# Performance work log

Measured on AMD Instinct MI355X. Metric: run time of the kernel, lower is better.

The kernel has to match this reference:

```python
import jax, jax.numpy as jnp
import numpy as np

EMB = 1024
HEADS = 16
HD = EMB // HEADS

def setup_inputs() -> dict:
    key = jax.random.key(0)
    ks = jax.random.split(key, 9)
    s = 1.0 / np.sqrt(EMB)
    x = jax.random.normal(ks[0], (4, 2048, EMB), dtype=jnp.float32)
    Wq = jax.random.uniform(ks[1], (EMB, EMB), jnp.float32, -s, s)
    bq = jax.random.uniform(ks[2], (EMB,), jnp.float32, -s, s)
    Wk = jax.random.uniform(ks[3], (EMB, EMB), jnp.float32, -s, s)
    bk = jax.random.uniform(ks[4], (EMB,), jnp.float32, -s, s)
    Wv = jax.random.uniform(ks[5], (EMB, EMB), jnp.float32, -s, s)
    bv = jax.random.uniform(ks[6], (EMB,), jnp.float32, -s, s)
    Wo = jax.random.uniform(ks[7], (EMB, EMB), jnp.float32, -s, s)
    bo = jax.random.uniform(ks[8], (EMB,), jnp.float32, -s, s)
    return {"x": x, "Wq": Wq, "bq": bq, "Wk": Wk, "bk": bk, "Wv": Wv, "bv": bv, "Wo": Wo, "bo": bo}

def reference(x, Wq, bq, Wk, bk, Wv, bv, Wo, bo):
    B, T, C = x.shape
    # projections (torch Linear: y = x @ W^T + b)
    q = (x @ Wq.T + bq).reshape(B, T, HEADS, HD).transpose(0, 2, 1, 3)  # [B,H,T,hd]
    k = (x @ Wk.T + bk).reshape(B, T, HEADS, HD).transpose(0, 2, 1, 3)
    v = (x @ Wv.T + bv).reshape(B, T, HEADS, HD).transpose(0, 2, 1, 3)
    scores = jnp.einsum('bhqd,bhkd->bhqk', q, k) / jnp.sqrt(jnp.float32(HD))
    weights = jax.nn.softmax(scores, axis=-1)
    attn = jnp.einsum('bhqk,bhkd->bhqd', weights, v)
    out = attn.transpose(0, 2, 1, 3).reshape(B, T, C)
    return out @ Wo.T + bo
```

## Files before the change

kernel.cpp:

```cpp
#include <hip/hip_runtime.h>

#define TSEQ  2048
#define BATCH 4
#define NHEAD 16
#define EMB   1024

typedef __attribute__((ext_vector_type(8))) __bf16 bf16x8;
typedef __attribute__((ext_vector_type(4))) __bf16 bf16x4;
typedef __attribute__((ext_vector_type(4))) float  floatx4;

__device__ __forceinline__ void gload_lds16(const __bf16* g, __bf16* lds_uniform_base) {
  __builtin_amdgcn_global_load_lds(
      (__attribute__((address_space(1))) void*)(g),
      (__attribute__((address_space(3))) void*)(lds_uniform_base),
      16, 0, 0);
}

__global__ __launch_bounds__(256) void cvt_f32_bf16(
    const float* __restrict__ src, __bf16* __restrict__ dst)
{
  const int gid = (blockIdx.x * 256 + threadIdx.x) * 4;
  const float4 v = *(const float4*)(src + gid);
  dst[gid + 0] = (__bf16)v.x;
  dst[gid + 1] = (__bf16)v.y;
  dst[gid + 2] = (__bf16)v.z;
  dst[gid + 3] = (__bf16)v.w;
}

__global__ __launch_bounds__(256) void cvt_w4(
    const float* __restrict__ s0, const float* __restrict__ s1,
    const float* __restrict__ s2, const float* __restrict__ s3,
    __bf16* __restrict__ d0, __bf16* __restrict__ d1,
    __bf16* __restrict__ d2, __bf16* __restrict__ d3)
{
  const int z = blockIdx.z;
  const float* src = (z == 0) ? s0 : (z == 1) ? s1 : (z == 2) ? s2 : s3;
  __bf16*      dst = (z == 0) ? d0 : (z == 1) ? d1 : (z == 2) ? d2 : d3;
  const int gid = (blockIdx.x * 256 + threadIdx.x) * 4;
  const float4 v = *(const float4*)(src + gid);
  dst[gid + 0] = (__bf16)v.x;
  dst[gid + 1] = (__bf16)v.y;
  dst[gid + 2] = (__bf16)v.z;
  dst[gid + 3] = (__bf16)v.w;
}

__global__ __launch_bounds__(256) void gemm_bt_bias(
    const __bf16* __restrict__ A,
    const __bf16* __restrict__ W0, const __bf16* __restrict__ W1, const __bf16* __restrict__ W2,
    const float* __restrict__ B0, const float* __restrict__ B1, const float* __restrict__ B2,
    __bf16* __restrict__ C0, __bf16* __restrict__ C1, __bf16* __restrict__ C2)
{
  const int z = blockIdx.z;
  const __bf16* W  = (z == 0) ? W0 : ((z == 1) ? W1 : W2);
  const float*  Bb = (z == 0) ? B0 : ((z == 1) ? B1 : B2);
  __bf16*       C  = (z == 0) ? C0 : ((z == 1) ? C1 : C2);
  const float  scl = (z == 0) ? 0.125f * 1.44269504088896340736f : 1.0f;

  const int tid  = threadIdx.x;
  const int lane = tid & 63;
  const int wid  = tid >> 6;
  const int l16  = lane & 15;
  const int quad = lane >> 4;
  const int wm   = wid & 1;
  const int wn   = wid >> 1;
  const int m0   = blockIdx.y * 128;
  const int n0   = blockIdx.x * 128;

  __shared__ alignas(16) __bf16 As[128 * 32];
  __shared__ alignas(16) __bf16 Bs[128 * 32];

  floatx4 acc[4][4];
#pragma unroll
  for (int i = 0; i < 4; i++)
#pragma unroll
    for (int j = 0; j < 4; j++) acc[i][j] = (floatx4){0.f, 0.f, 0.f, 0.f};

  const int srow = tid >> 2;
  const int sseg = tid & 3;

  for (int k0 = 0; k0 < 1024; k0 += 32) {
    __syncthreads();
#pragma unroll
    for (int is = 0; is < 2; is++) {
      const int row = is * 64 + srow;
      gload_lds16(A + (size_t)(m0 + row) * 1024 + k0 + sseg * 8,
                  &As[(is * 256 + wid * 64) * 8]);
      gload_lds16(W + (size_t)(n0 + row) * 1024 + k0 + sseg * 8,
                  &Bs[(is * 256 + wid * 64) * 8]);
    }
    __syncthreads();

    bf16x8 af[4], bfr[4];
#pragma unroll
    for (int i = 0; i < 4; i++) {
      af[i]  = *(const bf16x8*)(&As[(wm * 64 + i * 16 + l16) * 32 + quad * 8]);
      bfr[i] = *(const bf16x8*)(&Bs[(wn * 64 + i * 16 + l16) * 32 + quad * 8]);
    }
#pragma unroll
    for (int i = 0; i < 4; i++)
#pragma unroll
      for (int j = 0; j < 4; j++)
        acc[i][j] = __builtin_amdgcn_mfma_f32_16x16x32_bf16(af[i], bfr[j], acc[i][j], 0, 0, 0);
  }

  float bv[4];
#pragma unroll
  for (int j = 0; j < 4; j++) bv[j] = Bb[n0 + wn * 64 + j * 16 + l16];

#pragma unroll
  for (int i = 0; i < 4; i++) {
    const size_t mrow = (size_t)m0 + wm * 64 + i * 16 + quad * 4;
#pragma unroll
    for (int j = 0; j < 4; j++) {
      const int col = n0 + wn * 64 + j * 16 + l16;
#pragma unroll
      for (int r = 0; r < 4; r++)
        C[(mrow + r) * 1024 + col] = (__bf16)((acc[i][j][r] + bv[j]) * scl);
    }
  }
}

__global__ __launch_bounds__(256) void gemm_bt_bias_f32(
    const __bf16* __restrict__ A, const __bf16* __restrict__ W,
    const float* __restrict__ Bb, float* __restrict__ C)
{
  const int tid  = threadIdx.x;
  const int lane = tid & 63;
  const int wid  = tid >> 6;
  const int l16  = lane & 15;
  const int quad = lane >> 4;
  const int wm   = wid & 1;
  const int wn   = wid >> 1;
  const int m0   = blockIdx.y * 128;
  const int n0   = blockIdx.x * 128;

  __shared__ alignas(16) __bf16 As[128 * 32];
  __shared__ alignas(16) __bf16 Bs[128 * 32];

  floatx4 acc[4][4];
#pragma unroll
  for (int i = 0; i < 4; i++)
#pragma unroll
    for (int j = 0; j < 4; j++) acc[i][j] = (floatx4){0.f, 0.f, 0.f, 0.f};

  const int srow = tid >> 2;
  const int sseg = tid & 3;

  for (int k0 = 0; k0 < 1024; k0 += 32) {
    __syncthreads();
#pragma unroll
    for (int is = 0; is < 2; is++) {
      const int row = is * 64 + srow;
      gload_lds16(A + (size_t)(m0 + row) * 1024 + k0 + sseg * 8,
                  &As[(is * 256 + wid * 64) * 8]);
      gload_lds16(W + (size_t)(n0 + row) * 1024 + k0 + sseg * 8,
                  &Bs[(is * 256 + wid * 64) * 8]);
    }
    __syncthreads();

    bf16x8 af[4], bfr[4];
#pragma unroll
    for (int i = 0; i < 4; i++) {
      af[i]  = *(const bf16x8*)(&As[(wm * 64 + i * 16 + l16) * 32 + quad * 8]);
      bfr[i] = *(const bf16x8*)(&Bs[(wn * 64 + i * 16 + l16) * 32 + quad * 8]);
    }
#pragma unroll
    for (int i = 0; i < 4; i++)
#pragma unroll
      for (int j = 0; j < 4; j++)
        acc[i][j] = __builtin_amdgcn_mfma_f32_16x16x32_bf16(af[i], bfr[j], acc[i][j], 0, 0, 0);
  }

  float bv[4];
#pragma unroll
  for (int j = 0; j < 4; j++) bv[j] = Bb[n0 + wn * 64 + j * 16 + l16];

#pragma unroll
  for (int i = 0; i < 4; i++) {
    const size_t mrow = (size_t)m0 + wm * 64 + i * 16 + quad * 4;
#pragma unroll
    for (int j = 0; j < 4; j++) {
      const int col = n0 + wn * 64 + j * 16 + l16;
#pragma unroll
      for (int r = 0; r < 4; r++)
        C[(mrow + r) * 1024 + col] = acc[i][j][r] + bv[j];
    }
  }
}

__global__ __launch_bounds__(256) void v_transpose(
    const __bf16* __restrict__ V, __bf16* __restrict__ VT)
{
  const int t0 = blockIdx.x * 64;
  const int bh = blockIdx.y;
  const int b  = bh >> 4;
  const int h  = bh & 15;
  const int tid = threadIdx.x;

  __shared__ alignas(16) __bf16 Ls[64 * 72];

  const int row = tid >> 2, seg = tid & 3;
  const __bf16* src = V + ((size_t)(b * TSEQ + t0 + row)) * EMB + h * 64;
  *(bf16x8*)(&Ls[row * 72 + seg * 8])       = *(const bf16x8*)(src + seg * 8);
  *(bf16x8*)(&Ls[row * 72 + (seg + 4) * 8]) = *(const bf16x8*)(src + (seg + 4) * 8);
  __syncthreads();

  const int od = tid >> 2, oseg = tid & 3;
  bf16x8 o0, o1;
#pragma unroll
  for (int j = 0; j < 8; j++) o0[j] = Ls[(oseg * 16 + j) * 72 + od];
#pragma unroll
  for (int j = 0; j < 8; j++) o1[j] = Ls[(oseg * 16 + 8 + j) * 72 + od];
  __bf16* dst = VT + ((size_t)bh * 64 + od) * TSEQ + t0 + oseg * 16;
  *(bf16x8*)(dst)     = o0;
  *(bf16x8*)(dst + 8) = o1;
}

#define FA_STEP(BUF, WRPTR, DO_WR, DO_LD, LDTILE)                                        \
  {                                                                                      \
    if (DO_WR) *(bf16x8*)(WRPTR) = sv;                                                   \
    if (DO_LD) sv = *(const bf16x8*)(sptr0 + (size_t)(LDTILE) * sstep);                  \
    _Pragma("unroll")                                                                    \
    for (int kg = 0; kg < 2; kg++) {                                                     \
      const bf16x8 kf0 = *(const bf16x8*)(&Ks[BUF][(kg * 16 + l16) * 72 + quad * 8]);    \
      const bf16x8 kf1 = *(const bf16x8*)(&Ks[BUF][(kg * 16 + l16) * 72 + 32 + quad * 8]); \
      floatx4 t = (floatx4){0.f, 0.f, 0.f, 0.f};                                         \
      t = __builtin_amdgcn_mfma_f32_16x16x32_bf16(kf0, qf[0], t, 0, 0, 0);               \
      t = __builtin_amdgcn_mfma_f32_16x16x32_bf16(kf1, qf[1], t, 0, 0, 0);               \
      bf16x4 pk;                                                                         \
      float ps = 0.f;                                                                    \
      _Pragma("unroll")                                                                  \
      for (int r = 0; r < 4; r++) {                                                      \
        const float p = __builtin_amdgcn_exp2f(t[r]);                                    \
        ps += p;                                                                         \
        pk[r] = (__bf16)p;                                                               \
      }                                                                                  \
      l_r += ps;                                                                         \
      *(bf16x4*)(&Pb[wid][l16 * 40 + kg * 16 + quad * 4]) = pk;                          \
    }                                                                                    \
    __asm__ __volatile__("s_waitcnt lgkmcnt(0)" ::: "memory");                           \
    {                                                                                    \
      const bf16x8 pf = *(const bf16x8*)(&Pb[wid][l16 * 40 + quad * 8]);                 \
      _Pragma("unroll")                                                                  \
      for (int dg = 0; dg < 4; dg++) {                                                   \
        const bf16x8 vf = *(const bf16x8*)(&VTs[BUF][(dg * 16 + l16) * 40 + quad * 8]);  \
        Oacc[dg] = __builtin_amdgcn_mfma_f32_16x16x32_bf16(vf, pf, Oacc[dg], 0, 0, 0);   \
      }                                                                                  \
    }                                                                                    \
    __syncthreads();                                                                     \
  }

__global__ __launch_bounds__(512, 8) void flash_attn(
    const __bf16* __restrict__ Q, const __bf16* __restrict__ K,
    const __bf16* __restrict__ VT, __bf16* __restrict__ O)
{
  const int qt   = blockIdx.x;
  const int bh   = blockIdx.y;
  const int b    = bh >> 4;
  const int h    = bh & 15;
  const int tid  = threadIdx.x;
  const int wid  = tid >> 6;
  const int lane = tid & 63;
  const int l16  = lane & 15;
  const int quad = lane >> 4;

  __shared__ alignas(16) __bf16 Ks[2][32 * 72];
  __shared__ alignas(16) __bf16 VTs[2][64 * 40];
  __shared__ alignas(16) __bf16 Pb[8][16 * 40];

  const size_t base = ((size_t)b * TSEQ) * EMB + (size_t)h * 64;
  const __bf16* qptr  = Q + base;
  const __bf16* kptr  = K + base;
  const __bf16* vtptr = VT + (size_t)bh * 64 * TSEQ;
  __bf16*       optr  = O + base;

  const int qb = qt * 128 + wid * 16;

  bf16x8 qf[2];
#pragma unroll
  for (int hf = 0; hf < 2; hf++)
    qf[hf] = *(const bf16x8*)(qptr + (size_t)(qb + l16) * EMB + hf * 32 + quad * 8);

  floatx4 Oacc[4];
#pragma unroll
  for (int dg = 0; dg < 4; dg++) Oacc[dg] = (floatx4){0.f, 0.f, 0.f, 0.f};
  float l_r = 0.f;

  const bool isK = (tid < 256);
  const int t2   = tid & 255;
  const int krow = t2 >> 3, kseg = t2 & 7;
  const int vd   = t2 >> 2, vseg = t2 & 3;

  const __bf16* sptr0;
  size_t sstep;
  __bf16 *wr0, *wr1;
  if (isK) {
    sptr0 = kptr + (size_t)krow * EMB + kseg * 8;
    sstep = (size_t)32 * EMB;
    wr0 = &Ks[0][krow * 72 + kseg * 8];
    wr1 = &Ks[1][krow * 72 + kseg * 8];
  } else {
    sptr0 = vtptr + (size_t)vd * TSEQ + vseg * 8;
    sstep = 32;
    wr0 = &VTs[0][vd * 40 + vseg * 8];
    wr1 = &VTs[1][vd * 40 + vseg * 8];
  }

  bf16x8 sv = *(const bf16x8*)(sptr0);
  *(bf16x8*)wr0 = sv;
  sv = *(const bf16x8*)(sptr0 + sstep);
  __syncthreads();

  for (int kt = 0; kt < TSEQ / 32; kt += 2) {
    FA_STEP(0, wr1, true,                  kt + 2 < TSEQ / 32, kt + 2);
    FA_STEP(1, wr0, kt + 2 < TSEQ / 32,    kt + 3 < TSEQ / 32, kt + 3);
  }

  float l = l_r;
  l += __shfl_xor(l, 16);
  l += __shfl_xor(l, 32);
  const float inv = 1.0f / l;
#pragma unroll
  for (int dg = 0; dg < 4; dg++) {
    bf16x4 ov;
#pragma unroll
    for (int r = 0; r < 4; r++) ov[r] = (__bf16)(Oacc[dg][r] * inv);
    *(bf16x4*)(optr + (size_t)(qb + l16) * EMB + dg * 16 + quad * 4) = ov;
  }
}

extern "C" void kernel_launch(void* const* d_in, const int* in_sizes, int n_in,
                              void* d_out, int out_size, void* d_ws, size_t ws_size,
                              hipStream_t stream) {
  const float* x  = (const float*)d_in[0];
  const float* Wq = (const float*)d_in[1];
  const float* bq = (const float*)d_in[2];
  const float* Wk = (const float*)d_in[3];
  const float* bk = (const float*)d_in[4];
  const float* Wv = (const float*)d_in[5];
  const float* bv = (const float*)d_in[6];
  const float* Wo = (const float*)d_in[7];
  const float* bo = (const float*)d_in[8];
  float* out = (float*)d_out;

  const size_t NELEM = (size_t)BATCH * TSEQ * EMB;
  const size_t WELEM = (size_t)EMB * EMB;

  __bf16* q_b  = (__bf16*)d_out;
  __bf16* k_b  = q_b + NELEM;
  __bf16* x_b  = (__bf16*)d_ws;
  __bf16* v_b  = x_b + NELEM;
  __bf16* wq_b = v_b + NELEM;
  __bf16* wk_b = wq_b + WELEM;
  __bf16* wv_b = wk_b + WELEM;
  __bf16* wo_b = wv_b + WELEM;

  dim3 blk(256, 1, 1);

  cvt_f32_bf16<<<(int)(NELEM / 1024), blk, 0, stream>>>(x, x_b);
  cvt_w4<<<dim3((int)(WELEM / 1024), 1, 4), blk, 0, stream>>>(
      Wq, Wk, Wv, Wo, wq_b, wk_b, wv_b, wo_b);

  gemm_bt_bias<<<dim3(8, 64, 3), blk, 0, stream>>>(
      x_b, wq_b, wk_b, wv_b, bq, bk, bv, q_b, k_b, v_b);

  v_transpose<<<dim3(TSEQ / 64, BATCH * NHEAD), blk, 0, stream>>>(v_b, x_b);

  flash_attn<<<dim3(TSEQ / 128, BATCH * NHEAD), dim3(512, 1, 1), 0, stream>>>(
      q_b, k_b, x_b, v_b);

  gemm_bt_bias_f32<<<dim3(8, 64, 1), blk, 0, stream>>>(v_b, wo_b, bo, out);
}
```

Baseline: 315.0 us.

## Double KV tile to 64 and pass P through permlane swaps instead of LDS

Each loop step now covers 64 keys instead of 32. That halves the number of barriers and lets every thread stage one K and one V^T vector per tile. The softmax probabilities are no longer written to a per-wave LDS buffer and read back. Instead, permlane32/permlane16 swaps rearrange the score accumulator layout in registers into the B-operand fragment for the PV MFMA. s_setprio is raised around the compute section. The LDS round trip and its lgkmcnt wait are gone, in exchange for larger tiles and more register pressure under launch bounds of 512 threads and 8 waves.

Result: slower. 428.2 us (+35.9%).

```diff
diff --git a/kernel.cpp b/kernel.cpp
--- a/kernel.cpp
+++ b/kernel.cpp
@@ -8,6 +8,8 @@
 typedef __attribute__((ext_vector_type(8))) __bf16 bf16x8;
 typedef __attribute__((ext_vector_type(4))) __bf16 bf16x4;
 typedef __attribute__((ext_vector_type(4))) float  floatx4;
+typedef __attribute__((ext_vector_type(2))) unsigned int uint32x2;
+typedef __attribute__((ext_vector_type(4))) unsigned int uint32x4;
 
 __device__ __forceinline__ void gload_lds16(const __bf16* g, __bf16* lds_uniform_base) {
   __builtin_amdgcn_global_load_lds(
@@ -216,38 +218,65 @@
   *(bf16x8*)(dst + 8) = o1;
 }
 
-#define FA_STEP(BUF, WRPTR, DO_WR, DO_LD, LDTILE)                                        \
-  {                                                                                      \
-    if (DO_WR) *(bf16x8*)(WRPTR) = sv;                                                   \
-    if (DO_LD) sv = *(const bf16x8*)(sptr0 + (size_t)(LDTILE) * sstep);                  \
-    _Pragma("unroll")                                                                    \
-    for (int kg = 0; kg < 2; kg++) {                                                     \
-      const bf16x8 kf0 = *(const bf16x8*)(&Ks[BUF][(kg * 16 + l16) * 72 + quad * 8]);    \
-      const bf16x8 kf1 = *(const bf16x8*)(&Ks[BUF][(kg * 16 + l16) * 72 + 32 + quad * 8]); \
-      floatx4 t = (floatx4){0.f, 0.f, 0.f, 0.f};                                         \
-      t = __builtin_amdgcn_mfma_f32_16x16x32_bf16(kf0, qf[0], t, 0, 0, 0);               \
-      t = __builtin_amdgcn_mfma_f32_16x16x32_bf16(kf1, qf[1], t, 0, 0, 0);               \
-      bf16x4 pk;                                                                         \
-      float ps = 0.f;                                                                    \
-      _Pragma("unroll")                                                                  \
-      for (int r = 0; r < 4; r++) {                                                      \
-        const float p = __builtin_amdgcn_exp2f(t[r]);                                    \
-        ps += p;                                                                         \
-        pk[r] = (__bf16)p;                                                               \
-      }                                                                                  \
-      l_r += ps;                                                                         \
-      *(bf16x4*)(&Pb[wid][l16 * 40 + kg * 16 + quad * 4]) = pk;                          \
-    }                                                                                    \
-    __asm__ __volatile__("s_waitcnt lgkmcnt(0)" ::: "memory");                           \
-    {                                                                                    \
-      const bf16x8 pf = *(const bf16x8*)(&Pb[wid][l16 * 40 + quad * 8]);                 \
-      _Pragma("unroll")                                                                  \
-      for (int dg = 0; dg < 4; dg++) {                                                   \
-        const bf16x8 vf = *(const bf16x8*)(&VTs[BUF][(dg * 16 + l16) * 40 + quad * 8]);  \
-        Oacc[dg] = __builtin_amdgcn_mfma_f32_16x16x32_bf16(vf, pf, Oacc[dg], 0, 0, 0);   \
-      }                                                                                  \
-    }                                                                                    \
-    __syncthreads();                                                                     \
+#define KVB 64
+#define NT  (TSEQ / KVB)
+
+#define FA_STEP(BUF, KT)                                                                  \
+  {                                                                                       \
+    if ((KT) + 1 < NT) {                                                                  \
+      *(bf16x8*)(&Ks[(BUF) ^ 1][soff])  = kv;                                             \
+      *(bf16x8*)(&VTs[(BUF) ^ 1][soff]) = vv;                                             \
+    }                                                                                     \
+    if ((KT) + 2 < NT) {                                                                  \
+      kv = *(const bf16x8*)(ksrc + (size_t)((KT) + 2) * KVB * EMB);                       \
+      vv = *(const bf16x8*)(vsrc + ((KT) + 2) * KVB);                                     \
+    }                                                                                     \
+    bf16x8 pfrag[2];                                                                      \
+    __builtin_amdgcn_s_setprio(1);                                                        \
+    _Pragma("unroll")                                                                     \
+    for (int ks = 0; ks < 2; ks++) {                                                      \
+      const bf16x8 ka0 = *(const bf16x8*)(&Ks[BUF][((2 * ks) * 16 + l16) * 72 + quad * 8]);      \
+      const bf16x8 ka1 = *(const bf16x8*)(&Ks[BUF][((2 * ks) * 16 + l16) * 72 + 32 + quad * 8]); \
+      const bf16x8 kb0 = *(const bf16x8*)(&Ks[BUF][((2 * ks + 1) * 16 + l16) * 72 + quad * 8]);  \
+      const bf16x8 kb1 = *(const bf16x8*)(&Ks[BUF][((2 * ks + 1) * 16 + l16) * 72 + 32 + quad * 8]); \
+      floatx4 ta = (floatx4){0.f, 0.f, 0.f, 0.f};                                         \
+      floatx4 tb = (floatx4){0.f, 0.f, 0.f, 0.f};                                         \
+      ta = __builtin_amdgcn_mfma_f32_16x16x32_bf16(ka0, qf[0], ta, 0, 0, 0);              \
+      ta = __builtin_amdgcn_mfma_f32_16x16x32_bf16(ka1, qf[1], ta, 0, 0, 0);              \
+      tb = __builtin_amdgcn_mfma_f32_16x16x32_bf16(kb0, qf[0], tb, 0, 0, 0);              \
+      tb = __builtin_amdgcn_mfma_f32_16x16x32_bf16(kb1, qf[1], tb, 0, 0, 0);              \
+      bf16x4 pa, pb;                                                                      \
+      float ps = 0.f;                                                                     \
+      _Pragma("unroll")                                                                   \
+      for (int r = 0; r < 4; r++) {                                                       \
+        const float e = __builtin_amdgcn_exp2f(ta[r]);                                    \
+        ps += e; pa[r] = (__bf16)e;                                                       \
+      }                                                                                   \
+      _Pragma("unroll")                                                                   \
+      for (int r = 0; r < 4; r++) {                                                       \
+        const float e = __builtin_amdgcn_exp2f(tb[r]);                                    \
+        ps += e; pb[r] = (__bf16)e;                                                       \
+      }                                                                                   \
+      l_r += ps;                                                                          \
+      const uint32x2 A2 = __builtin_bit_cast(uint32x2, pa);                               \
+      const uint32x2 B2 = __builtin_bit_cast(uint32x2, pb);                               \
+      const uint32x2 r0 = __builtin_amdgcn_permlane32_swap(A2.x, B2.x, false, false);     \
+      const uint32x2 r1 = __builtin_amdgcn_permlane32_swap(A2.y, B2.y, false, false);     \
+      const uint32x2 s0 = __builtin_amdgcn_permlane16_swap(r0.x, r0.y, false, false);     \
+      const uint32x2 s1 = __builtin_amdgcn_permlane16_swap(r1.x, r1.y, false, false);     \
+      const uint32x4 fw = (uint32x4){s0.x, s1.x, s0.y, s1.y};                             \
+      pfrag[ks] = __builtin_bit_cast(bf16x8, fw);                                         \
+    }                                                                                     \
+    _Pragma("unroll")                                                                     \
+    for (int dg = 0; dg < 4; dg++) {                                                      \
+      _Pragma("unroll")                                                                   \
+      for (int ks = 0; ks < 2; ks++) {                                                    \
+        const bf16x8 vf = *(const bf16x8*)(&VTs[BUF][(dg * 16 + l16) * 72 + ks * 32 + quad * 8]); \
+        Oacc[dg] = __builtin_amdgcn_mfma_f32_16x16x32_bf16(vf, pfrag[ks], Oacc[dg], 0, 0, 0);     \
+      }                                                                                   \
+    }                                                                                     \
+    __builtin_amdgcn_s_setprio(0);                                                        \
+    __syncthreads();                                                                      \
   }
 
 __global__ __launch_bounds__(512, 8) void flash_attn(
@@ -264,9 +293,8 @@
   const int l16  = lane & 15;
   const int quad = lane >> 4;
 
-  __shared__ alignas(16) __bf16 Ks[2][32 * 72];
-  __shared__ alignas(16) __bf16 VTs[2][64 * 40];
-  __shared__ alignas(16) __bf16 Pb[8][16 * 40];
+  __shared__ alignas(16) __bf16 Ks[2][KVB * 72];
+  __shared__ alignas(16) __bf16 VTs[2][64 * 72];
 
   const size_t base = ((size_t)b * TSEQ) * EMB + (size_t)h * 64;
   const __bf16* qptr  = Q + base;
@@ -286,34 +314,23 @@
   for (int dg = 0; dg < 4; dg++) Oacc[dg] = (floatx4){0.f, 0.f, 0.f, 0.f};
   float l_r = 0.f;
 
-  const bool isK = (tid < 256);
-  const int t2   = tid & 255;
-  const int krow = t2 >> 3, kseg = t2 & 7;
-  const int vd   = t2 >> 2, vseg = t2 & 3;
-
-  const __bf16* sptr0;
-  size_t sstep;
-  __bf16 *wr0, *wr1;
-  if (isK) {
-    sptr0 = kptr + (size_t)krow * EMB + kseg * 8;
-    sstep = (size_t)32 * EMB;
-    wr0 = &Ks[0][krow * 72 + kseg * 8];
-    wr1 = &Ks[1][krow * 72 + kseg * 8];
-  } else {
-    sptr0 = vtptr + (size_t)vd * TSEQ + vseg * 8;
-    sstep = 32;
-    wr0 = &VTs[0][vd * 40 + vseg * 8];
-    wr1 = &VTs[1][vd * 40 + vseg * 8];
-  }
-
-  bf16x8 sv = *(const bf16x8*)(sptr0);
-  *(bf16x8*)wr0 = sv;
-  sv = *(const bf16x8*)(sptr0 + sstep);
+  const int srow = tid >> 3, sseg = tid & 7;
+  const __bf16* ksrc = kptr  + (size_t)srow * EMB  + sseg * 8;
+  const __bf16* vsrc = vtptr + (size_t)srow * TSEQ + sseg * 8;
+  const int soff = srow * 72 + sseg * 8;
+
+  bf16x8 kv = *(const bf16x8*)(ksrc);
+  bf16x8 vv = *(const bf16x8*)(vsrc);
+  *(bf16x8*)(&Ks[0][soff])  = kv;
+  *(bf16x8*)(&VTs[0][soff]) = vv;
+  kv = *(const bf16x8*)(ksrc + (size_t)KVB * EMB);
+  vv = *(const bf16x8*)(vsrc + KVB);
   __syncthreads();
 
-  for (int kt = 0; kt < TSEQ / 32; kt += 2) {
-    FA_STEP(0, wr1, true,                  kt + 2 < TSEQ / 32, kt + 2);
-    FA_STEP(1, wr0, kt + 2 < TSEQ / 32,    kt + 3 < TSEQ / 32, kt + 3);
+#pragma unroll 1
+  for (int kt = 0; kt < NT; kt += 2) {
+    FA_STEP(0, kt);
+    FA_STEP(1, kt + 1);
   }
 
   float l = l_r;
```
